# Kernel tuning notes

Measured on AMD Instinct MI355X. Metric: run time of the kernel, lower is better.

The kernel has to match this reference:

```python
import jax, jax.numpy as jnp
import numpy as np

N = 4096  # square [B, T+1] as required by original indexing (T = shape[0], indexed on dim 1)
GAMMA = 0.99

def setup_inputs() -> dict:
    key = jax.random.key(0)
    ks = jax.random.split(key, 6)
    shape = (N, N)
    names = ["Q", "expected_target_Q", "target_Q", "rewards",
             "target_policy_probs", "behaviour_policy_probs"]
    return {n: jax.random.normal(k, shape, dtype=jnp.float32) for n, k in zip(names, ks)}

def _retrace_loss(Q, expected_target_Q, target_Q, rewards,
                  target_policy_probs, behaviour_policy_probs):
    rewards = rewards * 100.0
    # retrace weights c_t = exp(min(log pi - log b, 0)) = min(1, pi/b)
    c_ret = jnp.exp(jnp.minimum(target_policy_probs - behaviour_policy_probs, 0.0))
    T = Q.shape[0]  # faithful to original (square inputs => equals time length)
    last = target_Q[:, T - 1]  # Q_ret[:, -1] = target_Q[:, -1]
    # reverse-time linear recurrence via a single scan:
    # Q_ret[t-1] = r[t-1] + gamma*c[t]*(Q_ret[t] - target_Q[t]) + gamma*E[t]
    xs = (rewards[:, :T - 1].T[::-1],          # [T-1, B], t-1 = T-2 .. 0
          c_ret[:, 1:T].T[::-1],               # c[t],  t = T-1 .. 1
          target_Q[:, 1:T].T[::-1],
          expected_target_Q[:, 1:T].T[::-1])

    def step(q_next, x):
        r, c, tq, eq = x
        q = r + GAMMA * c * (q_next - tq) + GAMMA * eq
        return q, q

    _, qs = jax.lax.scan(step, last, xs)       # qs: [T-1, B] for t = T-2 .. 0
    Q_ret = jnp.concatenate([qs[::-1].T, last[:, None]], axis=1)  # [B, T]
    Q_ret = jax.lax.stop_gradient(Q_ret)       # computed under torch.no_grad()
    return jnp.mean((Q - Q_ret) ** 2)

def reference(Q, expected_target_Q, target_Q, rewards,
              target_policy_probs, behaviour_policy_probs):
    return _retrace_loss(Q, expected_target_Q, target_Q, rewards,
                         target_policy_probs, behaviour_policy_probs)
```

## Files before the change

kernel.cpp:

```cpp
#include <hip/hip_runtime.h>


#define NROWS 4096
#define TLEN  4096
#define CHUNK 256
#define NCHUNK (TLEN / CHUNK)
#define BLOCK 256
#define WPB   (BLOCK / 64)

__global__ __launch_bounds__(BLOCK) void retrace_main(
    const float* __restrict__ Q,
    const float* __restrict__ eQ,
    const float* __restrict__ tQ,
    const float* __restrict__ rw,
    const float* __restrict__ tpp,
    const float* __restrict__ bpp,
    double* __restrict__ partials)
{
    constexpr float G = 0.99f;
    const int lane = threadIdx.x & 63;
    const int row  = blockIdx.x * WPB + (threadIdx.x >> 6);
    const long long base = (long long)row * TLEN;

    const int ua0 = (TLEN - 4) - 4 * lane;

    float4 cR  = *(const float4*)(rw  + base + ua0);
    float4 cT  = *(const float4*)(tpp + base + ua0);
    float4 cP  = *(const float4*)(bpp + base + ua0);
    float4 cQt = *(const float4*)(tQ  + base + ua0);
    float4 cE  = *(const float4*)(eQ  + base + ua0);
    float4 cQm = *(const float4*)(Q   + base + ua0);

    float y_state = 0.0f;
    float acc     = 0.0f;
    float pTx = 0.f, pPx = 0.f, pQtx = 0.f, pEx = 0.f;

    #pragma unroll 1
    for (int c = 0; c < NCHUNK; ++c) {
        float4 nR, nT, nP, nQt, nE, nQm;
        if (c + 1 < NCHUNK) {
            const int uan = ua0 - (c + 1) * CHUNK;
            nR  = *(const float4*)(rw  + base + uan);
            nT  = *(const float4*)(tpp + base + uan);
            nP  = *(const float4*)(bpp + base + uan);
            nQt = *(const float4*)(tQ  + base + uan);
            nE  = *(const float4*)(eQ  + base + uan);
            nQm = *(const float4*)(Q   + base + uan);
        }

        float t4v = __shfl_up(cT.x,  1, 64);
        float p4v = __shfl_up(cP.x,  1, 64);
        float q4v = __shfl_up(cQt.x, 1, 64);
        float e4v = __shfl_up(cE.x,  1, 64);
        const float bT = __shfl(pTx,  63, 64);
        const float bP = __shfl(pPx,  63, 64);
        const float bQ = __shfl(pQtx, 63, 64);
        const float bE = __shfl(pEx,  63, 64);
        if (lane == 0 && c > 0) { t4v = bT; p4v = bP; q4v = bQ; e4v = bE; }

        const float rv[4] = {cR.x,  cR.y,  cR.z,  cR.w};
        const float tv[4] = {cT.x,  cT.y,  cT.z,  cT.w};
        const float pv[4] = {cP.x,  cP.y,  cP.z,  cP.w};
        const float qv[4] = {cQt.x, cQt.y, cQt.z, cQt.w};
        const float ev[4] = {cE.x,  cE.y,  cE.z,  cE.w};
        const float qm[4] = {cQm.x, cQm.y, cQm.z, cQm.w};

        float Aa[4], Bb[4];
        #pragma unroll
        for (int m = 1; m <= 3; ++m) {
            const float cr = __expf(fminf(tv[m] - pv[m], 0.0f));
            const float gc = G * cr;
            Aa[m - 1] = gc;
            Bb[m - 1] = fmaf(100.0f, rv[m - 1], fmaf(-gc, qv[m], G * ev[m]));
        }
        if (c == 0 && lane == 0) {
            Aa[3] = 0.0f;
            Bb[3] = qv[3];
        } else {
            const float cr = __expf(fminf(t4v - p4v, 0.0f));
            const float gc = G * cr;
            Aa[3] = gc;
            Bb[3] = fmaf(100.0f, rv[3], fmaf(-gc, q4v, G * e4v));
        }

        float Ac = 1.0f, Bc = 0.0f;
        #pragma unroll
        for (int k = 0; k < 4; ++k) {
            const int idx = 3 - k;
            Bc = fmaf(Aa[idx], Bc, Bb[idx]);
            Ac = Aa[idx] * Ac;
        }

        float Ai = Ac, Bi = Bc;
        #pragma unroll
        for (int off = 1; off < 64; off <<= 1) {
            const float Ap = __shfl_up(Ai, off, 64);
            const float Bp = __shfl_up(Bi, off, 64);
            if (lane >= off) {
                Bi = fmaf(Ai, Bp, Bi);
                Ai = Ai * Ap;
            }
        }

        float Ae = __shfl_up(Ai, 1, 64);
        float Be = __shfl_up(Bi, 1, 64);
        if (lane == 0) { Ae = 1.0f; Be = 0.0f; }
        float y = fmaf(Ae, y_state, Be);

        #pragma unroll
        for (int k = 0; k < 4; ++k) {
            const int idx = 3 - k;
            y = fmaf(Aa[idx], y, Bb[idx]);
            const float d = qm[idx] - y;
            acc = fmaf(d, d, acc);
        }

        const float A63 = __shfl(Ai, 63, 64);
        const float B63 = __shfl(Bi, 63, 64);
        y_state = fmaf(A63, y_state, B63);

        pTx = cT.x; pPx = cP.x; pQtx = cQt.x; pEx = cE.x;
        cR = nR; cT = nT; cP = nP; cQt = nQt; cE = nE; cQm = nQm;
    }

    #pragma unroll
    for (int off = 32; off > 0; off >>= 1)
        acc += __shfl_down(acc, off, 64);
    if (lane == 0)
        partials[row] = (double)acc;
}

__global__ __launch_bounds__(256) void retrace_finalize(
    const double* __restrict__ partials, float* __restrict__ out)
{
    __shared__ double sRed[4];
    double s = 0.0;
    for (int i = threadIdx.x; i < NROWS; i += 256) s += partials[i];
    #pragma unroll
    for (int off = 32; off > 0; off >>= 1)
        s += __shfl_down(s, off, 64);
    if ((threadIdx.x & 63) == 0) sRed[threadIdx.x >> 6] = s;
    __syncthreads();
    if (threadIdx.x == 0) {
        const double tot = sRed[0] + sRed[1] + sRed[2] + sRed[3];
        out[0] = (float)(tot / ((double)NROWS * (double)TLEN));
    }
}

extern "C" void kernel_launch(void* const* d_in, const int* in_sizes, int n_in,
                              void* d_out, int out_size, void* d_ws, size_t ws_size,
                              hipStream_t stream)
{
    const float* Q   = (const float*)d_in[0];
    const float* eQ  = (const float*)d_in[1];
    const float* tQ  = (const float*)d_in[2];
    const float* rw  = (const float*)d_in[3];
    const float* tpp = (const float*)d_in[4];
    const float* bpp = (const float*)d_in[5];
    double* partials = (double*)d_ws;

    retrace_main<<<NROWS / WPB, BLOCK, 0, stream>>>(Q, eQ, tQ, rw, tpp, bpp, partials);
    retrace_finalize<<<1, 256, 0, stream>>>(partials, (float*)d_out);
}
```

Measured before the change: 345.7 us.

## Split each row's scan across two waves and resolve chunk carries in a second pass

Each row is now handled by two wavefronts of eight chunks each. Every chunk writes its affine transfer (A, B) and three quadratic loss moments to a workspace, so its loss can be evaluated later for any incoming carry. A new resolve kernel walks the chunks in reverse for each row, chaining carries and summing y-dependent losses. This doubles the number of waves and shortens the serial chain per wave to improve memory-level parallelism. In exchange it adds an extra kernel launch, workspace traffic, and per-chunk wave reductions, and the expanded quadratic loss form may lose float precision.

```diff
diff --git a/kernel.cpp b/kernel.cpp
--- a/kernel.cpp
+++ b/kernel.cpp
@@ -4,59 +4,72 @@
 #define NROWS 4096
 #define TLEN  4096
 #define CHUNK 256
-#define NCHUNK (TLEN / CHUNK)
+#define CPR   (TLEN / CHUNK)
 #define BLOCK 256
-#define WPB   (BLOCK / 64)
-
-__global__ __launch_bounds__(BLOCK) void retrace_main(
+#define CPW   8
+#define GRID_A (NROWS * CPR / CPW * 64 / BLOCK)
+
+#define WS_PLANES (CPR * 5)
+
+__global__ __launch_bounds__(BLOCK) void retrace_stream(
     const float* __restrict__ Q,
     const float* __restrict__ eQ,
     const float* __restrict__ tQ,
     const float* __restrict__ rw,
     const float* __restrict__ tpp,
     const float* __restrict__ bpp,
-    double* __restrict__ partials)
+    float* __restrict__ ws)
 {
     constexpr float G = 0.99f;
     const int lane = threadIdx.x & 63;
-    const int row  = blockIdx.x * WPB + (threadIdx.x >> 6);
+    const int wid  = blockIdx.x * (BLOCK / 64) + (threadIdx.x >> 6);
+    const int row  = wid >> 1;
+    const int c0   = (wid & 1) * CPW;
     const long long base = (long long)row * TLEN;
 
-    const int ua0 = (TLEN - 4) - 4 * lane;
-
-    float4 cR  = *(const float4*)(rw  + base + ua0);
-    float4 cT  = *(const float4*)(tpp + base + ua0);
-    float4 cP  = *(const float4*)(bpp + base + ua0);
-    float4 cQt = *(const float4*)(tQ  + base + ua0);
-    float4 cE  = *(const float4*)(eQ  + base + ua0);
-    float4 cQm = *(const float4*)(Q   + base + ua0);
-
-    float y_state = 0.0f;
-    float acc     = 0.0f;
-    float pTx = 0.f, pPx = 0.f, pQtx = 0.f, pEx = 0.f;
+    long long off = base + (long long)c0 * CHUNK + 4 * lane;
+    float4 cR  = *(const float4*)(rw  + off);
+    float4 cT  = *(const float4*)(tpp + off);
+    float4 cP  = *(const float4*)(bpp + off);
+    float4 cQt = *(const float4*)(tQ  + off);
+    float4 cE  = *(const float4*)(eQ  + off);
+    float4 cQm = *(const float4*)(Q   + off);
+    float cbT = 0.f, cbP = 0.f, cbQ = 0.f, cbE = 0.f;
+    {
+        const int tn = c0 * CHUNK + CHUNK;
+        if (tn < TLEN) {
+            cbT = tpp[base + tn]; cbP = bpp[base + tn];
+            cbQ = tQ [base + tn]; cbE = eQ [base + tn];
+        }
+    }
 
     #pragma unroll 1
-    for (int c = 0; c < NCHUNK; ++c) {
+    for (int k = 0; k < CPW; ++k) {
+        const int c = c0 + k;
+
         float4 nR, nT, nP, nQt, nE, nQm;
-        if (c + 1 < NCHUNK) {
-            const int uan = ua0 - (c + 1) * CHUNK;
-            nR  = *(const float4*)(rw  + base + uan);
-            nT  = *(const float4*)(tpp + base + uan);
-            nP  = *(const float4*)(bpp + base + uan);
-            nQt = *(const float4*)(tQ  + base + uan);
-            nE  = *(const float4*)(eQ  + base + uan);
-            nQm = *(const float4*)(Q   + base + uan);
-        }
-
-        float t4v = __shfl_up(cT.x,  1, 64);
-        float p4v = __shfl_up(cP.x,  1, 64);
-        float q4v = __shfl_up(cQt.x, 1, 64);
-        float e4v = __shfl_up(cE.x,  1, 64);
-        const float bT = __shfl(pTx,  63, 64);
-        const float bP = __shfl(pPx,  63, 64);
-        const float bQ = __shfl(pQtx, 63, 64);
-        const float bE = __shfl(pEx,  63, 64);
-        if (lane == 0 && c > 0) { t4v = bT; p4v = bP; q4v = bQ; e4v = bE; }
+        float nbT = 0.f, nbP = 0.f, nbQ = 0.f, nbE = 0.f;
+        if (k + 1 < CPW) {
+            const long long noff = base + (long long)(c + 1) * CHUNK + 4 * lane;
+            nR  = *(const float4*)(rw  + noff);
+            nT  = *(const float4*)(tpp + noff);
+            nP  = *(const float4*)(bpp + noff);
+            nQt = *(const float4*)(tQ  + noff);
+            nE  = *(const float4*)(eQ  + noff);
+            nQm = *(const float4*)(Q   + noff);
+            const int tn = (c + 1) * CHUNK + CHUNK;
+            if (tn < TLEN) {
+                nbT = tpp[base + tn]; nbP = bpp[base + tn];
+                nbQ = tQ [base + tn]; nbE = eQ [base + tn];
+            }
+        }
+
+        float t3 = __shfl_down(cT.x,  1, 64);
+        float p3 = __shfl_down(cP.x,  1, 64);
+        float q3 = __shfl_down(cQt.x, 1, 64);
+        float e3 = __shfl_down(cE.x,  1, 64);
+        const bool top = (lane == 63);
+        if (top) { t3 = cbT; p3 = cbP; q3 = cbQ; e3 = cbE; }
 
         const float rv[4] = {cR.x,  cR.y,  cR.z,  cR.w};
         const float tv[4] = {cT.x,  cT.y,  cT.z,  cT.w};
@@ -65,69 +78,93 @@
         const float ev[4] = {cE.x,  cE.y,  cE.z,  cE.w};
         const float qm[4] = {cQm.x, cQm.y, cQm.z, cQm.w};
 
-        float Aa[4], Bb[4];
-        #pragma unroll
-        for (int m = 1; m <= 3; ++m) {
-            const float cr = __expf(fminf(tv[m] - pv[m], 0.0f));
+        float A[4], B[4];
+        #pragma unroll
+        for (int j = 0; j < 3; ++j) {
+            const float cr = __expf(fminf(tv[j+1] - pv[j+1], 0.0f));
             const float gc = G * cr;
-            Aa[m - 1] = gc;
-            Bb[m - 1] = fmaf(100.0f, rv[m - 1], fmaf(-gc, qv[m], G * ev[m]));
-        }
-        if (c == 0 && lane == 0) {
-            Aa[3] = 0.0f;
-            Bb[3] = qv[3];
+            A[j] = gc;
+            B[j] = fmaf(100.0f, rv[j], fmaf(-gc, qv[j+1], G * ev[j+1]));
+        }
+        if (top && c == CPR - 1) {
+            A[3] = 0.0f;
+            B[3] = qv[3];
         } else {
-            const float cr = __expf(fminf(t4v - p4v, 0.0f));
+            const float cr = __expf(fminf(t3 - p3, 0.0f));
             const float gc = G * cr;
-            Aa[3] = gc;
-            Bb[3] = fmaf(100.0f, rv[3], fmaf(-gc, q4v, G * e4v));
-        }
-
-        float Ac = 1.0f, Bc = 0.0f;
-        #pragma unroll
-        for (int k = 0; k < 4; ++k) {
-            const int idx = 3 - k;
-            Bc = fmaf(Aa[idx], Bc, Bb[idx]);
-            Ac = Aa[idx] * Ac;
-        }
-
-        float Ai = Ac, Bi = Bc;
-        #pragma unroll
-        for (int off = 1; off < 64; off <<= 1) {
-            const float Ap = __shfl_up(Ai, off, 64);
-            const float Bp = __shfl_up(Bi, off, 64);
-            if (lane >= off) {
-                Bi = fmaf(Ai, Bp, Bi);
-                Ai = Ai * Ap;
+            A[3] = gc;
+            B[3] = fmaf(100.0f, rv[3], fmaf(-gc, q3, G * e3));
+        }
+
+        float CA[4], CB[4];
+        CA[3] = A[3];            CB[3] = B[3];
+        CA[2] = A[2] * CA[3];    CB[2] = fmaf(A[2], CB[3], B[2]);
+        CA[1] = A[1] * CA[2];    CB[1] = fmaf(A[1], CB[2], B[1]);
+        CA[0] = A[0] * CA[1];    CB[0] = fmaf(A[0], CB[1], B[0]);
+
+        float SA = CA[0], SB = CB[0];
+        #pragma unroll
+        for (int o = 1; o < 64; o <<= 1) {
+            const float nA = __shfl_down(SA, o, 64);
+            const float nB = __shfl_down(SB, o, 64);
+            if (lane + o < 64) {
+                SB = fmaf(SA, nB, SB);
+                SA = SA * nA;
             }
         }
-
-        float Ae = __shfl_up(Ai, 1, 64);
-        float Be = __shfl_up(Bi, 1, 64);
-        if (lane == 0) { Ae = 1.0f; Be = 0.0f; }
-        float y = fmaf(Ae, y_state, Be);
-
-        #pragma unroll
-        for (int k = 0; k < 4; ++k) {
-            const int idx = 3 - k;
-            y = fmaf(Aa[idx], y, Bb[idx]);
-            const float d = qm[idx] - y;
-            acc = fmaf(d, d, acc);
-        }
-
-        const float A63 = __shfl(Ai, 63, 64);
-        const float B63 = __shfl(Bi, 63, 64);
-        y_state = fmaf(A63, y_state, B63);
-
-        pTx = cT.x; pPx = cP.x; pQtx = cQt.x; pEx = cE.x;
+        float EA = __shfl_down(SA, 1, 64);
+        float EB = __shfl_down(SB, 1, 64);
+        if (top) { EA = 1.0f; EB = 0.0f; }
+
+        float s0 = 0.f, s1 = 0.f, s2 = 0.f;
+        #pragma unroll
+        for (int j = 0; j < 4; ++j) {
+            const float cA = CA[j] * EA;
+            const float cB = fmaf(CA[j], EB, CB[j]);
+            const float P  = qm[j] - cB;
+            s0 = fmaf(cA, cA, s0);
+            s1 = fmaf(P,  cA, s1);
+            s2 = fmaf(P,  P,  s2);
+        }
+        #pragma unroll
+        for (int o = 32; o > 0; o >>= 1) {
+            s0 += __shfl_down(s0, o, 64);
+            s1 += __shfl_down(s1, o, 64);
+            s2 += __shfl_down(s2, o, 64);
+        }
+
+        if (lane == 0) {
+            float* w = ws + (size_t)(c * 5) * NROWS + row;
+            w[0 * NROWS] = SA;
+            w[1 * NROWS] = SB;
+            w[2 * NROWS] = s0;
+            w[3 * NROWS] = s1;
+            w[4 * NROWS] = s2;
+        }
+
         cR = nR; cT = nT; cP = nP; cQt = nQt; cE = nE; cQm = nQm;
-    }
-
+        cbT = nbT; cbP = nbP; cbQ = nbQ; cbE = nbE;
+    }
+}
+
+__global__ __launch_bounds__(BLOCK) void retrace_resolve(
+    const float* __restrict__ ws, double* __restrict__ partials)
+{
+    const int row = blockIdx.x * BLOCK + threadIdx.x;
+    float y = 0.0f;
+    double loss = 0.0;
     #pragma unroll
-    for (int off = 32; off > 0; off >>= 1)
-        acc += __shfl_down(acc, off, 64);
-    if (lane == 0)
-        partials[row] = (double)acc;
+    for (int c = CPR - 1; c >= 0; --c) {
+        const float* w = ws + (size_t)(c * 5) * NROWS + row;
+        const float Ac = w[0 * NROWS];
+        const float Bc = w[1 * NROWS];
+        const float s0 = w[2 * NROWS];
+        const float s1 = w[3 * NROWS];
+        const float s2 = w[4 * NROWS];
+        loss += (double)fmaf(fmaf(s0, y, -2.0f * s1), y, s2);
+        y = fmaf(Ac, y, Bc);
+    }
+    partials[row] = loss;
 }
 
 __global__ __launch_bounds__(256) void retrace_finalize(
@@ -157,8 +194,11 @@
     const float* rw  = (const float*)d_in[3];
     const float* tpp = (const float*)d_in[4];
     const float* bpp = (const float*)d_in[5];
-    double* partials = (double*)d_ws;
-
-    retrace_main<<<NROWS / WPB, BLOCK, 0, stream>>>(Q, eQ, tQ, rw, tpp, bpp, partials);
+
+    float*  ws       = (float*)d_ws;
+    double* partials = (double*)(ws + (size_t)WS_PLANES * NROWS);
+
+    retrace_stream<<<GRID_A, BLOCK, 0, stream>>>(Q, eQ, tQ, rw, tpp, bpp, ws);
+    retrace_resolve<<<NROWS / BLOCK, BLOCK, 0, stream>>>(ws, partials);
     retrace_finalize<<<1, 256, 0, stream>>>(partials, (float*)d_out);
 }
```

Result: slower. 353.1 us (+2.1%).
